# Kernel tuning notes

Measured on AMD Instinct MI355X. Metric: run time of the kernel, lower is better.

Reference implementation:

```python
import jax, jax.numpy as jnp
import numpy as np

N, E, T, D, A = 16384, 65536, 2048, 64, 6


def _w(k, shape, fan_in):
    return jax.random.normal(k, shape, jnp.float32) / np.sqrt(fan_in)


def setup_inputs() -> dict:
    key = jax.random.key(0)
    ks = jax.random.split(key, 20)
    inp = {}
    inp["x"] = jax.random.normal(ks[0], (N, 3), jnp.float32)
    inp["edge_attr"] = jax.random.normal(ks[1], (E, 7), jnp.float32)
    inp["edge_index"] = jax.random.randint(ks[2], (2, E), 0, N)
    inp["nonring"] = jax.random.randint(ks[3], (T, 4), 0, N)
    inp["hx"] = jnp.zeros((1, D), jnp.float32)
    inp["cx"] = jnp.zeros((1, D), jnp.float32)
    inp["W_lin0"] = _w(ks[4], (D, 3), 3); inp["b_lin0"] = jnp.zeros((D,), jnp.float32)
    inp["W_e1"] = _w(ks[5], (128, 7), 7); inp["b_e1"] = jnp.zeros((128,), jnp.float32)
    inp["W_e2"] = _w(ks[6], (D * D, 128), 128); inp["b_e2"] = jnp.zeros((D * D,), jnp.float32)
    inp["conv_root"] = _w(ks[7], (D, D), D); inp["conv_bias"] = jnp.zeros((D,), jnp.float32)
    inp["gru_Wih"] = _w(ks[8], (3 * D, D), D); inp["gru_Whh"] = _w(ks[9], (3 * D, D), D)
    inp["gru_bih"] = jnp.zeros((3 * D,), jnp.float32); inp["gru_bhh"] = jnp.zeros((3 * D,), jnp.float32)
    inp["s2s_Wih"] = _w(ks[10], (4 * D, 2 * D), 2 * D); inp["s2s_Whh"] = _w(ks[11], (4 * D, D), D)
    inp["s2s_bih"] = jnp.zeros((4 * D,), jnp.float32); inp["s2s_bhh"] = jnp.zeros((4 * D,), jnp.float32)
    inp["mem_Wih"] = _w(ks[12], (4 * D, 2 * D), 2 * D); inp["mem_Whh"] = _w(ks[13], (4 * D, D), D)
    inp["mem_bih"] = jnp.zeros((4 * D,), jnp.float32); inp["mem_bhh"] = jnp.zeros((4 * D,), jnp.float32)
    inp["W_lin1"] = _w(ks[14], (D, 5 * D), 5 * D); inp["b_lin1"] = jnp.zeros((D,), jnp.float32)
    inp["W_lin2"] = _w(ks[15], (A, D), D); inp["b_lin2"] = jnp.zeros((A,), jnp.float32)
    inp["W_lin3"] = _w(ks[16], (1, 3 * D), 3 * D); inp["b_lin3"] = jnp.zeros((1,), jnp.float32)
    return inp


def _lstm_cell(xin, h, c, Wih, Whh, bih, bhh):
    g = xin @ Wih.T + bih + h @ Whh.T + bhh
    i, f, gg, o = jnp.split(g, 4, axis=-1)  # torch gate order i,f,g,o
    c = jax.nn.sigmoid(f) * c + jax.nn.sigmoid(i) * jnp.tanh(gg)
    h = jax.nn.sigmoid(o) * jnp.tanh(c)
    return h, c


def _gru_cell(xin, h, Wih, Whh, bih, bhh):
    gi = xin @ Wih.T + bih
    gh = h @ Whh.T + bhh
    ir, iz, inn = jnp.split(gi, 3, axis=-1)  # torch gate order r,z,n
    hr, hz, hn = jnp.split(gh, 3, axis=-1)
    r = jax.nn.sigmoid(ir + hr)
    z = jax.nn.sigmoid(iz + hz)
    n = jnp.tanh(inn + r * hn)
    return (1.0 - z) * n + z * h


def reference(x, edge_attr, edge_index, nonring, hx, cx,
              W_lin0, b_lin0, W_e1, b_e1, W_e2, b_e2, conv_root, conv_bias,
              gru_Wih, gru_Whh, gru_bih, gru_bhh,
              s2s_Wih, s2s_Whh, s2s_bih, s2s_bhh,
              mem_Wih, mem_Whh, mem_bih, mem_bhh,
              W_lin1, b_lin1, W_lin2, b_lin2, W_lin3, b_lin3):
    src, tgt = edge_index[0], edge_index[1]
    out = jax.nn.relu(x @ W_lin0.T + b_lin0)  # [N, D]
    h = out  # GRU hidden (nodes as batch)
    # edge-conditioned dim x dim matrices (NNConv edge MLP)
    ew = jax.nn.relu(edge_attr @ W_e1.T + b_e1)
    ew = (ew @ W_e2.T + b_e2).reshape(E, D, D)  # [E, D, D]
    cnt = jnp.maximum(jax.ops.segment_sum(jnp.ones((E,), out.dtype), tgt, num_segments=N), 1.0)
    for _ in range(3):
        msg = jnp.einsum('ed,edf->ef', out[src], ew)  # per-edge small matmul
        aggr = jax.ops.segment_sum(msg, tgt, num_segments=N) / cnt[:, None]  # scatter-mean
        m = jax.nn.relu(aggr + out @ conv_root + conv_bias)  # NNConv root + bias, then relu
        h = _gru_cell(m, h, gru_Wih, gru_Whh, gru_bih, gru_bhh)
        out = h
    # Set2Set pooling (single graph, B=1), processing_steps=3
    hs = jnp.zeros((1, D), out.dtype)
    cs = jnp.zeros((1, D), out.dtype)
    q_star = jnp.zeros((1, 2 * D), out.dtype)
    for _ in range(3):
        hs, cs = _lstm_cell(q_star, hs, cs, s2s_Wih, s2s_Whh, s2s_bih, s2s_bhh)
        a = jax.nn.softmax(out @ hs[0])  # [N]
        r = (a[:, None] * out).sum(0, keepdims=True)  # [1, D]
        q_star = jnp.concatenate([hs, r], axis=1)
    pool = q_star  # [1, 2D]
    lstm_out, cx_new = _lstm_cell(pool, hx, cx, mem_Wih, mem_Whh, mem_bih, mem_bhh)
    hx_new = lstm_out
    # torsion head: index_select -> view(4*D, -1) -> permute(1,0)
    sel = out[nonring.reshape(-1)]  # [4T, D]
    tfeat = sel.reshape(4 * D, -1).T  # [T, 4D], faithful to torch view semantics
    rep = jnp.repeat(lstm_out.reshape(-1), T).reshape(T, D)  # torch repeat_interleave + view
    pf = jnp.concatenate([tfeat, rep], axis=1)  # [T, 5D]
    logits = jax.nn.relu(pf @ W_lin1.T + b_lin1) @ W_lin2.T + b_lin2  # [T, A]
    v = jnp.concatenate([pool, lstm_out], axis=1) @ W_lin3.T + b_lin3  # [1, 1]
    return logits, v, hx_new, cx_new
```

## Files before the change

kernel.cpp:

```cpp
#include <hip/hip_runtime.h>

#define cN 16384
#define cE 65536
#define cT 2048
#define CAP 78

typedef __attribute__((ext_vector_type(8))) short short8;
typedef __attribute__((ext_vector_type(4))) float f32x4;
typedef __attribute__((ext_vector_type(4))) unsigned u32x4;

__device__ __forceinline__ short f2bf(float f){
  unsigned u = __float_as_uint(f);
  u = (u + 0x7FFFu + ((u >> 16) & 1u)) >> 16;
  return (short)u;
}
__device__ __forceinline__ float bf2f(short s){
  return __uint_as_float(((unsigned)(unsigned short)s) << 16);
}
__device__ __forceinline__ unsigned cvtpk(float lo, float hi){
  unsigned r;
  asm("v_cvt_pk_bf16_f32 %0, %1, %2" : "=v"(r) : "v"(lo), "v"(hi));
  return r;
}
__device__ __forceinline__ float sigm(float x){ return 1.f / (1.f + __expf(-x)); }
__device__ __forceinline__ unsigned fenc(float f){
  unsigned u = __float_as_uint(f);
  return (u & 0x80000000u) ? ~u : (u | 0x80000000u);
}
__device__ __forceinline__ float fdec(unsigned u){
  u = (u & 0x80000000u) ? (u & 0x7FFFFFFFu) : ~u;
  return __uint_as_float(u);
}
__device__ __forceinline__ float wred(float v){
  v += __shfl_xor(v, 32); v += __shfl_xor(v, 16); v += __shfl_xor(v, 8);
  v += __shfl_xor(v, 4);  v += __shfl_xor(v, 2);  v += __shfl_xor(v, 1);
  return v;
}

__global__ __launch_bounds__(256) void k_lin0(const float* __restrict__ x,
    const float* __restrict__ W, const float* __restrict__ b, float* __restrict__ out)
{
  int i = blockIdx.x * 256 + threadIdx.x;
  int n = i >> 6, f = i & 63;
  float acc = b[f] + x[n*3]*W[f*3] + x[n*3+1]*W[f*3+1] + x[n*3+2]*W[f*3+2];
  out[i] = fmaxf(acc, 0.f);
}

__global__ __launch_bounds__(256) void k_h1(const float* __restrict__ ea,
    const float* __restrict__ W, const float* __restrict__ b, short* __restrict__ h1)
{
  int i = blockIdx.x * 256 + threadIdx.x;
  int e = i >> 7, k = i & 127;
  const float* a = ea + e * 7;
  const float* w = W + k * 7;
  float acc = b[k];
  #pragma unroll
  for (int c = 0; c < 7; c++) acc += a[c] * w[c];
  h1[i] = f2bf(fmaxf(acc, 0.f));
}

__global__ __launch_bounds__(256) void k_w2f(const float* __restrict__ W2, short* __restrict__ w2f)
{
  int o = blockIdx.x * 256 + threadIdx.x;
  int j = o & 7, l = (o >> 3) & 63, ks = (o >> 9) & 31, c = (o >> 14) & 7, fb = (o >> 17) & 3;
  int f = fb * 16 + (l & 15);
  int d = c * 8 + j;
  int k = ks * 4 + ((l >> 4) & 3);
  w2f[o] = f2bf(W2[(d * 64 + f) * 128 + k]);
}

__global__ __launch_bounds__(256) void k_b2f(const float* __restrict__ b2, short* __restrict__ b2f)
{
  int o = blockIdx.x * 256 + threadIdx.x;
  int j = o & 7, l = (o >> 3) & 63, ks2 = (o >> 9) & 1, fb = (o >> 10) & 3;
  int d = ks2 * 32 + ((l >> 4) & 3) * 8 + j;
  int f = fb * 16 + (l & 15);
  b2f[o] = f2bf(b2[d * 64 + f]);
}

__global__ __launch_bounds__(256) void k_wpack(const float* __restrict__ convW,
    const float* __restrict__ Wih, const float* __restrict__ Whh, short* __restrict__ wpk)
{
  int o = blockIdx.x * 256 + threadIdx.x;
  int j = o & 7, l = (o >> 3) & 63, kc = (o >> 9) & 1, cb = o >> 10;
  int k = kc * 32 + ((l >> 4) & 3) * 8 + j;
  int c16 = l & 15;
  float v;
  if (cb < 4)       v = convW[k * 64 + cb * 16 + c16];
  else if (cb < 16) v = Wih[((cb - 4) * 16 + c16) * 64 + k];
  else              v = Whh[((cb - 16) * 16 + c16) * 64 + k];
  wpk[o] = f2bf(v);
}

__global__ __launch_bounds__(256) void k_deg(const int* __restrict__ ei, int* __restrict__ deg)
{
  int e = blockIdx.x * 256 + threadIdx.x;
  atomicAdd(&deg[ei[cE + e]], 1);
}

__global__ __launch_bounds__(1024) void k_scan(const int* __restrict__ deg,
    int* __restrict__ rowp, float* __restrict__ cnt)
{
  __shared__ int part[1024];
  int tid = threadIdx.x;
  int base = tid * 16;
  int loc[16]; int s = 0;
  #pragma unroll
  for (int i = 0; i < 16; i++){ loc[i] = s; s += deg[base + i]; }
  part[tid] = s;
  __syncthreads();
  for (int off = 1; off < 1024; off <<= 1){
    int v = (tid >= off) ? part[tid - off] : 0;
    __syncthreads();
    part[tid] += v;
    __syncthreads();
  }
  int inc = part[tid];
  int eb = inc - s;
  #pragma unroll
  for (int i = 0; i < 16; i++){
    rowp[base + i] = eb + loc[i];
    int dv = deg[base + i];
    cnt[base + i] = (float)(dv > 0 ? dv : 1);
  }
  if (tid == 1023) rowp[16384] = inc;
}

__global__ __launch_bounds__(256) void k_scatter(const int* __restrict__ ei,
    const int* __restrict__ rowp, int* __restrict__ cur,
    int* __restrict__ esrc, int* __restrict__ eidx)
{
  int e = blockIdx.x * 256 + threadIdx.x;
  int t = ei[cE + e];
  int pos = rowp[t] + atomicAdd(&cur[t], 1);
  esrc[pos] = ei[e];
  eidx[pos] = e;
}

__global__ __launch_bounds__(256) void k_sagg(const float* __restrict__ out,
    const short* __restrict__ h1, const short* __restrict__ w2f,
    const short* __restrict__ b2f, const int* __restrict__ rowp,
    const int* __restrict__ esrc, const int* __restrict__ eidx,
    float* __restrict__ aggr)
{
  __shared__ __align__(16) short S[16][1040];
  __shared__ __align__(16) unsigned h1i[CAP][64];
  __shared__ __align__(16) float outsf[CAP][64];
  __shared__ __align__(16) short osb[16][72];
  int tid = threadIdx.x, w = tid >> 6, lane = tid & 63;
  int t0 = blockIdx.x * 16;

  int ebase = rowp[t0];
  int eend  = rowp[t0 + 16];
  int ecnt  = eend - ebase;
  bool fits = (ecnt <= CAP);
  int scnt  = fits ? ecnt : CAP;
  for (int i = w; i < scnt; i += 4){
    int eid = eidx[ebase + i];
    int src = esrc[ebase + i];
    unsigned lo = (unsigned short)h1[(size_t)eid * 128 + lane];
    unsigned hi = (unsigned short)h1[(size_t)eid * 128 + 64 + lane];
    h1i[i][lane] = lo | (hi << 16);
    outsf[i][lane] = out[(size_t)src * 64 + lane];
  }
  int toff[4], tcnt[4];
  #pragma unroll
  for (int g = 0; g < 4; g++){
    int t = t0 + w * 4 + g;
    int a = rowp[t], b = rowp[t + 1];
    toff[g] = a - ebase; tcnt[g] = b - a;
  }
  __syncthreads();

  #pragma unroll
  for (int g = 0; g < 4; g++){
    int ti = w * 4 + g;
    float os = 0.f;
    int tf = toff[g], tc = tcnt[g];
    for (int p = 0; p < tc; p++){
      int slot = tf + p;
      if (slot < CAP) os += outsf[slot][lane];
      else            os += out[(size_t)esrc[ebase + slot] * 64 + lane];
    }
    osb[ti][lane] = (short)cvtpk(os, os);
  }

  f32x4 acc = {0.f, 0.f, 0.f, 0.f};
  int arow = lane & 15, kg = lane >> 4;
  for (int c = 0; c < 8; ++c){
    #pragma unroll
    for (int g = 0; g < 4; ++g){
      int ti = w * 4 + g;
      float a0[8], a1[8];
      #pragma unroll
      for (int d = 0; d < 8; d++){ a0[d] = 0.f; a1[d] = 0.f; }
      int tc = tcnt[g], tf = toff[g];
      if (fits){
        #pragma unroll 2
        for (int p = 0; p < tc; ++p){
          int slot = tf + p;
          unsigned u = h1i[slot][lane];
          float h1a = __uint_as_float(u << 16);
          float h1b = __uint_as_float(u & 0xFFFF0000u);
          f32x4 o0 = *(const f32x4*)&outsf[slot][c * 8];
          f32x4 o1 = *(const f32x4*)&outsf[slot][c * 8 + 4];
          a0[0] = fmaf(o0[0], h1a, a0[0]); a1[0] = fmaf(o0[0], h1b, a1[0]);
          a0[1] = fmaf(o0[1], h1a, a0[1]); a1[1] = fmaf(o0[1], h1b, a1[1]);
          a0[2] = fmaf(o0[2], h1a, a0[2]); a1[2] = fmaf(o0[2], h1b, a1[2]);
          a0[3] = fmaf(o0[3], h1a, a0[3]); a1[3] = fmaf(o0[3], h1b, a1[3]);
          a0[4] = fmaf(o1[0], h1a, a0[4]); a1[4] = fmaf(o1[0], h1b, a1[4]);
          a0[5] = fmaf(o1[1], h1a, a0[5]); a1[5] = fmaf(o1[1], h1b, a1[5]);
          a0[6] = fmaf(o1[2], h1a, a0[6]); a1[6] = fmaf(o1[2], h1b, a1[6]);
          a0[7] = fmaf(o1[3], h1a, a0[7]); a1[7] = fmaf(o1[3], h1b, a1[7]);
        }
      } else {
        for (int p = 0; p < tc; ++p){
          int slot = tf + p;
          float h1a, h1b;
          if (slot < CAP){
            unsigned u = h1i[slot][lane];
            h1a = __uint_as_float(u << 16);
            h1b = __uint_as_float(u & 0xFFFF0000u);
            f32x4 o0 = *(const f32x4*)&outsf[slot][c * 8];
            f32x4 o1 = *(const f32x4*)&outsf[slot][c * 8 + 4];
            #pragma unroll
            for (int d = 0; d < 4; d++){
              a0[d] = fmaf(o0[d], h1a, a0[d]); a1[d] = fmaf(o0[d], h1b, a1[d]);
              a0[4+d] = fmaf(o1[d], h1a, a0[4+d]); a1[4+d] = fmaf(o1[d], h1b, a1[4+d]);
            }
          } else {
            int eid = eidx[ebase + slot];
            int src = esrc[ebase + slot];
            h1a = bf2f(h1[(size_t)eid * 128 + lane]);
            h1b = bf2f(h1[(size_t)eid * 128 + 64 + lane]);
            #pragma unroll
            for (int d = 0; d < 8; d++){
              float o = out[(size_t)src * 64 + c * 8 + d];
              a0[d] = fmaf(o, h1a, a0[d]); a1[d] = fmaf(o, h1b, a1[d]);
            }
          }
        }
      }
      u32x4 p0, p1;
      p0[0] = cvtpk(a0[0], a0[1]); p0[1] = cvtpk(a0[2], a0[3]);
      p0[2] = cvtpk(a0[4], a0[5]); p0[3] = cvtpk(a0[6], a0[7]);
      p1[0] = cvtpk(a1[0], a1[1]); p1[1] = cvtpk(a1[2], a1[3]);
      p1[2] = cvtpk(a1[4], a1[5]); p1[3] = cvtpk(a1[6], a1[7]);
      *(u32x4*)&S[ti][lane * 8]       = p0;
      *(u32x4*)&S[ti][512 + lane * 8] = p1;
    }
    __syncthreads();
    const short* bbase = w2f + ((size_t)(w * 8 + c) * 32) * 512 + lane * 8;
    #pragma unroll
    for (int ks = 0; ks < 32; ++ks){
      short8 afr = *(const short8*)&S[arow][ks * 32 + kg * 8];
      short8 bfr = *(const short8*)(bbase + (size_t)ks * 512);
      acc = __builtin_amdgcn_mfma_f32_16x16x32_bf16(afr, bfr, acc, 0, 0, 0);
    }
    __syncthreads();
  }
  #pragma unroll
  for (int ks2 = 0; ks2 < 2; ++ks2){
    short8 osf = *(const short8*)&osb[arow][ks2 * 32 + kg * 8];
    short8 bfr = *(const short8*)(b2f + ((size_t)((w * 2 + ks2) * 64 + lane)) * 8);
    acc = __builtin_amdgcn_mfma_f32_16x16x32_bf16(osf, bfr, acc, 0, 0, 0);
  }
  int fcol = w * 16 + arow;
  int trow = kg * 4;
  #pragma unroll
  for (int q = 0; q < 4; q++)
    aggr[(size_t)(t0 + trow + q) * 64 + fcol] = acc[q];
}

__global__ __launch_bounds__(256) void k_nodeM(float* __restrict__ out,
    const float* __restrict__ aggr, const float* __restrict__ cnt,
    const short* __restrict__ wpk, const float* __restrict__ convB,
    const float* __restrict__ bih, const float* __restrict__ bhh)
{
  __shared__ __align__(16) short outA[64][72];
  __shared__ __align__(16) short mA[64][72];
  __shared__ float sb[448];
  const short8* WF = (const short8*)wpk;
  int tid = threadIdx.x, w = tid >> 6, lane = tid & 63;
  int n0 = blockIdx.x * 64;
  for (int i = tid; i < 2048; i += 256){
    int r = i >> 5, c2 = (i & 31) * 2;
    float2 v = *(const float2*)&out[(size_t)(n0 + r) * 64 + c2];
    *(unsigned*)&outA[r][c2] = cvtpk(v.x, v.y);
  }
  if (tid < 64) sb[tid] = convB[tid];
  for (int i = tid; i < 192; i += 256){ sb[64 + i] = bih[i]; sb[256 + i] = bhh[i]; }
  __syncthreads();
  int arow = lane & 15, kg = lane >> 4;
  int r0 = w * 16;
  short8 aof0 = *(const short8*)&outA[r0 + arow][kg * 8];
  short8 aof1 = *(const short8*)&outA[r0 + arow][32 + kg * 8];
  float ic[4];
  #pragma unroll
  for (int q = 0; q < 4; q++)
    ic[q] = 1.0f / fmaxf(cnt[n0 + r0 + kg * 4 + q], 1.0f);
  #pragma unroll
  for (int cf = 0; cf < 4; cf++){
    f32x4 a = {0.f, 0.f, 0.f, 0.f};
    a = __builtin_amdgcn_mfma_f32_16x16x32_bf16(aof0, WF[(cf * 2 + 0) * 64 + lane], a, 0, 0, 0);
    a = __builtin_amdgcn_mfma_f32_16x16x32_bf16(aof1, WF[(cf * 2 + 1) * 64 + lane], a, 0, 0, 0);
    int col = cf * 16 + arow;
    float cb_ = sb[col];
    #pragma unroll
    for (int q = 0; q < 4; q++){
      int r = n0 + r0 + kg * 4 + q;
      float m = fmaxf(aggr[(size_t)r * 64 + col] * ic[q] + a[q] + cb_, 0.f);
      mA[r0 + kg * 4 + q][col] = f2bf(m);
    }
  }
  __syncthreads();
  short8 amf0 = *(const short8*)&mA[r0 + arow][kg * 8];
  short8 amf1 = *(const short8*)&mA[r0 + arow][32 + kg * 8];
  #pragma unroll
  for (int co = 0; co < 4; co++){
    f32x4 gir = {0,0,0,0}, giz = {0,0,0,0}, gin = {0,0,0,0};
    f32x4 ghr = {0,0,0,0}, ghz = {0,0,0,0}, ghn = {0,0,0,0};
    gir = __builtin_amdgcn_mfma_f32_16x16x32_bf16(amf0, WF[((4  + co) * 2 + 0) * 64 + lane], gir, 0, 0, 0);
    gir = __builtin_amdgcn_mfma_f32_16x16x32_bf16(amf1, WF[((4  + co) * 2 + 1) * 64 + lane], gir, 0, 0, 0);
    giz = __builtin_amdgcn_mfma_f32_16x16x32_bf16(amf0, WF[((8  + co) * 2 + 0) * 64 + lane], giz, 0, 0, 0);
    giz = __builtin_amdgcn_mfma_f32_16x16x32_bf16(amf1, WF[((8  + co) * 2 + 1) * 64 + lane], giz, 0, 0, 0);
    gin = __builtin_amdgcn_mfma_f32_16x16x32_bf16(amf0, WF[((12 + co) * 2 + 0) * 64 + lane], gin, 0, 0, 0);
    gin = __builtin_amdgcn_mfma_f32_16x16x32_bf16(amf1, WF[((12 + co) * 2 + 1) * 64 + lane], gin, 0, 0, 0);
    ghr = __builtin_amdgcn_mfma_f32_16x16x32_bf16(aof0, WF[((16 + co) * 2 + 0) * 64 + lane], ghr, 0, 0, 0);
    ghr = __builtin_amdgcn_mfma_f32_16x16x32_bf16(aof1, WF[((16 + co) * 2 + 1) * 64 + lane], ghr, 0, 0, 0);
    ghz = __builtin_amdgcn_mfma_f32_16x16x32_bf16(aof0, WF[((20 + co) * 2 + 0) * 64 + lane], ghz, 0, 0, 0);
    ghz = __builtin_amdgcn_mfma_f32_16x16x32_bf16(aof1, WF[((20 + co) * 2 + 1) * 64 + lane], ghz, 0, 0, 0);
    ghn = __builtin_amdgcn_mfma_f32_16x16x32_bf16(aof0, WF[((24 + co) * 2 + 0) * 64 + lane], ghn, 0, 0, 0);
    ghn = __builtin_amdgcn_mfma_f32_16x16x32_bf16(aof1, WF[((24 + co) * 2 + 1) * 64 + lane], ghn, 0, 0, 0);
    int col = co * 16 + arow;
    float bir = sb[64 + col],  biz = sb[128 + col], bin_ = sb[192 + col];
    float bhr = sb[256 + col], bhz = sb[320 + col], bhn = sb[384 + col];
    #pragma unroll
    for (int q = 0; q < 4; q++){
      size_t r = (size_t)(n0 + r0 + kg * 4 + q);
      float rr = sigm(gir[q] + bir + ghr[q] + bhr);
      float zz = sigm(giz[q] + biz + ghz[q] + bhz);
      float nn = tanhf(gin[q] + bin_ + rr * (ghn[q] + bhn));
      float o = out[r * 64 + col];
      out[r * 64 + col] = (1.f - zz) * nn + zz * o;
    }
  }
}

__global__ __launch_bounds__(256) void k_dotsF(const float* __restrict__ out,
    const float* __restrict__ Wih, const float* __restrict__ Whh,
    const float* __restrict__ bih, const float* __restrict__ bhh,
    float* __restrict__ scal, float* __restrict__ sbuf, int st)
{
  __shared__ float q[128];
  __shared__ float hsL[64];
  __shared__ float gsh[4][64];
  __shared__ float hsh[64];
  __shared__ float smax[4];
  const float* pg = scal + st * 256;
  float* pn = scal + (st + 1) * 256;
  int tid = threadIdx.x, gg = tid >> 6, lane = tid & 63;
  if (gg == 0){
    float hs = pg[lane];
    float es = pg[193];
    float rv = (es == 0.f) ? 0.f : pg[128 + lane] / es;
    q[lane] = hs; q[64 + lane] = rv; hsL[lane] = hs;
  }
  __syncthreads();
  float2 fq = *(const float2*)&q[2 * lane];
  float hv0 = hsL[lane];
  #pragma unroll 4
  for (int o = 0; o < 64; o++){
    int row = gg * 64 + o;
    float2 wv = *(const float2*)&Wih[(size_t)row * 128 + 2 * lane];
    float s = wv.x * fq.x + wv.y * fq.y + Whh[(size_t)row * 64 + lane] * hv0;
    s = wred(s);
    if (lane == 0) gsh[gg][o] = s;
  }
  __syncthreads();
  if (gg == 0){
    float gi = gsh[0][lane] + bih[lane]       + bhh[lane];
    float gf = gsh[1][lane] + bih[64 + lane]  + bhh[64 + lane];
    float gv = gsh[2][lane] + bih[128 + lane] + bhh[128 + lane];
    float go = gsh[3][lane] + bih[192 + lane] + bhh[192 + lane];
    float cs = pg[64 + lane];
    float cn = sigm(gf) * cs + sigm(gi) * tanhf(gv);
    float hn = sigm(go) * tanhf(cn);
    hsh[lane] = hn;
    if (blockIdx.x == 0){ pn[lane] = hn; pn[64 + lane] = cn; }
  }
  __syncthreads();
  int nbase = blockIdx.x * 64 + gg * 16;
  float hv = hsh[lane];
  float wmax = -3.4e38f;
  #pragma unroll 4
  for (int i = 0; i < 16; i++){
    int n = nbase + i;
    float p = wred(out[(size_t)n * 64 + lane] * hv);
    if (lane == 0) sbuf[n] = p;
    wmax = fmaxf(wmax, p);
  }
  if (lane == 0) smax[gg] = wmax;
  __syncthreads();
  if (tid == 0){
    float m = fmaxf(fmaxf(smax[0], smax[1]), fmaxf(smax[2], smax[3]));
    atomicMax((unsigned*)(pn + 192), fenc(m));
  }
}

__global__ __launch_bounds__(256) void k_smF(const float* __restrict__ out,
    const float* __restrict__ sbuf, float* __restrict__ scal, int st)
{
  float* pn = scal + (st + 1) * 256;
  __shared__ float ebuf[64];
  __shared__ float rpart[4][64];
  int tid = threadIdx.x, wid = tid >> 6, lane = tid & 63;
  float gm = fdec(((const unsigned*)pn)[192]);
  int n0 = blockIdx.x * 64;
  if (tid < 64) ebuf[tid] = __expf(sbuf[n0 + tid] - gm);
  __syncthreads();
  float racc = 0.f;
  #pragma unroll 4
  for (int i = 0; i < 16; i++){
    int idx = wid * 16 + i;
    racc += ebuf[idx] * out[(size_t)(n0 + idx) * 64 + lane];
  }
  rpart[wid][lane] = racc;
  __syncthreads();
  if (wid == 0){
    float rt = rpart[0][lane] + rpart[1][lane] + rpart[2][lane] + rpart[3][lane];
    atomicAdd(&pn[128 + lane], rt);
  } else if (wid == 1){
    float es = wred(ebuf[lane]);
    if (lane == 0) atomicAdd(&pn[193], es);
  }
}

__global__ __launch_bounds__(256) void k_memlstm(const float* __restrict__ Wih,
    const float* __restrict__ Whh, const float* __restrict__ bih,
    const float* __restrict__ bhh, const float* __restrict__ hx,
    const float* __restrict__ cx, const float* __restrict__ W3,
    const float* __restrict__ b3, float* __restrict__ scal, float* __restrict__ dout)
{
  __shared__ float pool[128];
  __shared__ float hxs[64];
  __shared__ float gsh[4][64];
  __shared__ float lob[64];
  const float* pg = scal + 3 * 256;
  int tid = threadIdx.x, gg = tid >> 6, lane = tid & 63;
  if (gg == 0){
    pool[lane] = pg[lane];
    pool[64 + lane] = pg[128 + lane] / pg[193];
    hxs[lane] = hx[lane];
  }
  __syncthreads();
  float2 fq = *(const float2*)&pool[2 * lane];
  float hv = hxs[lane];
  #pragma unroll 4
  for (int o = 0; o < 64; o++){
    int row = gg * 64 + o;
    float2 wv = *(const float2*)&Wih[(size_t)row * 128 + 2 * lane];
    float s = wv.x * fq.x + wv.y * fq.y + Whh[(size_t)row * 64 + lane] * hv;
    s = wred(s);
    if (lane == 0) gsh[gg][o] = s;
  }
  __syncthreads();
  if (gg == 0){
    float gi = gsh[0][lane] + bih[lane]       + bhh[lane];
    float gf = gsh[1][lane] + bih[64 + lane]  + bhh[64 + lane];
    float gv = gsh[2][lane] + bih[128 + lane] + bhh[128 + lane];
    float go = gsh[3][lane] + bih[192 + lane] + bhh[192 + lane];
    float cn = sigm(gf) * cx[lane] + sigm(gi) * tanhf(gv);
    float hn = sigm(go) * tanhf(cn);
    dout[12289 + lane] = hn;
    dout[12353 + lane] = cn;
    scal[1024 + lane] = hn;
    lob[lane] = hn;
  }
  __syncthreads();
  if (gg == 0){
    float a = pool[lane] * W3[lane] + pool[64 + lane] * W3[64 + lane]
            + lob[lane] * W3[128 + lane];
    a = wred(a);
    if (lane == 0) dout[12288] = a + b3[0];
  }
}

__global__ __launch_bounds__(256) void k_head(const float* __restrict__ out,
    const int* __restrict__ nr, const float* __restrict__ scal,
    const float* __restrict__ W1, const float* __restrict__ b1,
    const float* __restrict__ W2, const float* __restrict__ b2,
    float* __restrict__ dout)
{
  __shared__ float pf[4][320];
  __shared__ float hb[4][64];
  int tid = threadIdx.x, wid = tid >> 6, lane = tid & 63;
  int t = blockIdx.x * 4 + wid;
  float lo = scal[1024 + (t >> 5)];
  #pragma unroll
  for (int rep = 0; rep < 4; rep++){
    int j = rep * 64 + lane;
    int idx = nr[j * 32 + (t >> 6)];
    pf[wid][j] = out[idx * 64 + (t & 63)];
  }
  pf[wid][256 + lane] = lo;
  __syncthreads();
  float acc = b1[lane];
  const float* w = W1 + lane * 320;
  #pragma unroll 4
  for (int j = 0; j < 320; j++) acc += pf[wid][j] * w[j];
  hb[wid][lane] = fmaxf(acc, 0.f);
  __syncthreads();
  if (lane < 6){
    float a2 = b2[lane];
    const float* w2 = W2 + lane * 64;
    #pragma unroll 4
    for (int f = 0; f < 64; f++) a2 += hb[wid][f] * w2[f];
    dout[t * 6 + lane] = a2;
  }
}

extern "C" void kernel_launch(void* const* d_in, const int* in_sizes, int n_in,
                              void* d_out, int out_size, void* d_ws, size_t ws_size,
                              hipStream_t stream)
{
  const float* x         = (const float*)d_in[0];
  const float* edge_attr = (const float*)d_in[1];
  const int*   ei        = (const int*)d_in[2];
  const int*   nonring   = (const int*)d_in[3];
  const float* hx        = (const float*)d_in[4];
  const float* cx        = (const float*)d_in[5];
  const float* W_lin0 = (const float*)d_in[6];  const float* b_lin0 = (const float*)d_in[7];
  const float* W_e1   = (const float*)d_in[8];  const float* b_e1   = (const float*)d_in[9];
  const float* W_e2   = (const float*)d_in[10]; const float* b_e2   = (const float*)d_in[11];
  const float* convW  = (const float*)d_in[12]; const float* convB  = (const float*)d_in[13];
  const float* gWih   = (const float*)d_in[14]; const float* gWhh   = (const float*)d_in[15];
  const float* gbih   = (const float*)d_in[16]; const float* gbhh   = (const float*)d_in[17];
  const float* sWih   = (const float*)d_in[18]; const float* sWhh   = (const float*)d_in[19];
  const float* sbih   = (const float*)d_in[20]; const float* sbhh   = (const float*)d_in[21];
  const float* mWih   = (const float*)d_in[22]; const float* mWhh   = (const float*)d_in[23];
  const float* mbih   = (const float*)d_in[24]; const float* mbhh   = (const float*)d_in[25];
  const float* W_lin1 = (const float*)d_in[26]; const float* b_lin1 = (const float*)d_in[27];
  const float* W_lin2 = (const float*)d_in[28]; const float* b_lin2 = (const float*)d_in[29];
  const float* W_lin3 = (const float*)d_in[30]; const float* b_lin3 = (const float*)d_in[31];
  float* dout = (float*)d_out;

  char* w = (char*)d_ws;
  float* outb = (float*)w;  w += (size_t)cN * 64 * 4;
  float* aggr = (float*)w;  w += (size_t)cN * 64 * 4;
  short* h1   = (short*)w;  w += (size_t)cE * 128 * 2;
  short* w2f  = (short*)w;  w += (size_t)64 * 8192 * 2;
  short* b2f  = (short*)w;  w += 4096 * 2;
  short* wpk  = (short*)w;  w += 28672 * 2;
  float* cntb = (float*)w;  w += cN * 4;
  float* sbuf = (float*)w;  w += cN * 4;
  float* scal = (float*)w;  w += 1088 * 4;
  int* deg  = (int*)w;  w += cN * 4;
  int* cur  = (int*)w;  w += cN * 4;
  int* rowp = (int*)w;  w += (cN + 1) * 4 + 60;
  int* esrc = (int*)w;  w += cE * 4;
  int* eidx = (int*)w;  w += cE * 4;

  hipMemsetAsync(deg, 0, cN * 4, stream);
  hipMemsetAsync(cur, 0, cN * 4, stream);
  hipMemsetAsync(scal, 0, 1088 * 4, stream);

  k_lin0<<<cN * 64 / 256, 256, 0, stream>>>(x, W_lin0, b_lin0, outb);
  k_h1<<<cE * 128 / 256, 256, 0, stream>>>(edge_attr, W_e1, b_e1, h1);
  k_w2f<<<64 * 8192 / 256, 256, 0, stream>>>(W_e2, w2f);
  k_b2f<<<16, 256, 0, stream>>>(b_e2, b2f);
  k_wpack<<<112, 256, 0, stream>>>(convW, gWih, gWhh, wpk);
  k_deg<<<cE / 256, 256, 0, stream>>>(ei, deg);
  k_scan<<<1, 1024, 0, stream>>>(deg, rowp, cntb);
  k_scatter<<<cE / 256, 256, 0, stream>>>(ei, rowp, cur, esrc, eidx);

  for (int it = 0; it < 3; it++){
    k_sagg<<<cN / 16, 256, 0, stream>>>(outb, h1, w2f, b2f, rowp, esrc, eidx, aggr);
    k_nodeM<<<cN / 64, 256, 0, stream>>>(outb, aggr, cntb, wpk, convB, gbih, gbhh);
  }

  for (int st = 0; st < 3; st++){
    k_dotsF<<<cN / 64, 256, 0, stream>>>(outb, sWih, sWhh, sbih, sbhh, scal, sbuf, st);
    k_smF<<<cN / 64, 256, 0, stream>>>(outb, sbuf, scal, st);
  }

  k_memlstm<<<1, 256, 0, stream>>>(mWih, mWhh, mbih, mbhh, hx, cx, W_lin3, b_lin3, scal, dout);
  k_head<<<cT / 4, 256, 0, stream>>>(outb, nonring, scal, W_lin1, b_lin1, W_lin2, b_lin2, dout);
}
```

Before: 601.4 us.

## Double sagg tile with bf16 staged features; restructure set2set softmax as two-level reduction

k_sagg now processes 32 targets per block with 512 threads. It raises the LDS edge cache capacity and stores the gathered source features as packed bf16 to halve LDS use. The Set2Set softmax drops the global atomicMax plus second pass over node features. Each block now computes a local max, the exp-sum and the weighted partial sum from an LDS tile, and a single-block kernel rescales and combines the partials and, on the last step, runs the memory LSTM. This removes one full pass over the node features and the separate k_memlstm launch, at the cost of extra bf16 rounding of features in the aggregation and a serial single-block reduction.

```diff
diff --git a/kernel.cpp b/kernel.cpp
--- a/kernel.cpp
+++ b/kernel.cpp
@@ -3,7 +3,7 @@
 #define cN 16384
 #define cE 65536
 #define cT 2048
-#define CAP 78
+#define CAP 168
 
 typedef __attribute__((ext_vector_type(8))) short short8;
 typedef __attribute__((ext_vector_type(4))) float f32x4;
@@ -23,17 +23,15 @@
   return r;
 }
 __device__ __forceinline__ float sigm(float x){ return 1.f / (1.f + __expf(-x)); }
-__device__ __forceinline__ unsigned fenc(float f){
-  unsigned u = __float_as_uint(f);
-  return (u & 0x80000000u) ? ~u : (u | 0x80000000u);
-}
-__device__ __forceinline__ float fdec(unsigned u){
-  u = (u & 0x80000000u) ? (u & 0x7FFFFFFFu) : ~u;
-  return __uint_as_float(u);
-}
 __device__ __forceinline__ float wred(float v){
   v += __shfl_xor(v, 32); v += __shfl_xor(v, 16); v += __shfl_xor(v, 8);
   v += __shfl_xor(v, 4);  v += __shfl_xor(v, 2);  v += __shfl_xor(v, 1);
+  return v;
+}
+__device__ __forceinline__ float wredmax(float v){
+  v = fmaxf(v, __shfl_xor(v, 32)); v = fmaxf(v, __shfl_xor(v, 16));
+  v = fmaxf(v, __shfl_xor(v, 8));  v = fmaxf(v, __shfl_xor(v, 4));
+  v = fmaxf(v, __shfl_xor(v, 2));  v = fmaxf(v, __shfl_xor(v, 1));
   return v;
 }
 
@@ -137,31 +135,34 @@
   eidx[pos] = e;
 }
 
-__global__ __launch_bounds__(256) void k_sagg(const float* __restrict__ out,
+__global__ __launch_bounds__(512) void k_sagg(const float* __restrict__ out,
     const short* __restrict__ h1, const short* __restrict__ w2f,
     const short* __restrict__ b2f, const int* __restrict__ rowp,
     const int* __restrict__ esrc, const int* __restrict__ eidx,
     float* __restrict__ aggr)
 {
-  __shared__ __align__(16) short S[16][1040];
+  __shared__ __align__(16) short S[32][1040];
   __shared__ __align__(16) unsigned h1i[CAP][64];
-  __shared__ __align__(16) float outsf[CAP][64];
-  __shared__ __align__(16) short osb[16][72];
+  __shared__ __align__(16) unsigned outsp[CAP][32];
+  __shared__ __align__(16) short osb[32][72];
   int tid = threadIdx.x, w = tid >> 6, lane = tid & 63;
-  int t0 = blockIdx.x * 16;
+  int t0 = blockIdx.x * 32;
 
   int ebase = rowp[t0];
-  int eend  = rowp[t0 + 16];
+  int eend  = rowp[t0 + 32];
   int ecnt  = eend - ebase;
   bool fits = (ecnt <= CAP);
   int scnt  = fits ? ecnt : CAP;
-  for (int i = w; i < scnt; i += 4){
+  for (int i = w; i < scnt; i += 8){
     int eid = eidx[ebase + i];
     int src = esrc[ebase + i];
     unsigned lo = (unsigned short)h1[(size_t)eid * 128 + lane];
     unsigned hi = (unsigned short)h1[(size_t)eid * 128 + 64 + lane];
     h1i[i][lane] = lo | (hi << 16);
-    outsf[i][lane] = out[(size_t)src * 64 + lane];
+    if (lane < 32){
+      float2 v = *(const float2*)&out[(size_t)src * 64 + lane * 2];
+      outsp[i][lane] = cvtpk(v.x, v.y);
+    }
   }
   int toff[4], tcnt[4];
   #pragma unroll
@@ -179,14 +180,19 @@
     int tf = toff[g], tc = tcnt[g];
     for (int p = 0; p < tc; p++){
       int slot = tf + p;
-      if (slot < CAP) os += outsf[slot][lane];
-      else            os += out[(size_t)esrc[ebase + slot] * 64 + lane];
+      if (slot < CAP){
+        unsigned u = outsp[slot][lane >> 1];
+        os += __uint_as_float((lane & 1) ? (u & 0xFFFF0000u) : (u << 16));
+      } else {
+        os += out[(size_t)esrc[ebase + slot] * 64 + lane];
+      }
     }
     osb[ti][lane] = (short)cvtpk(os, os);
   }
 
   f32x4 acc = {0.f, 0.f, 0.f, 0.f};
   int arow = lane & 15, kg = lane >> 4;
+  int rb = w >> 2, fb = w & 3;
   for (int c = 0; c < 8; ++c){
     #pragma unroll
     for (int g = 0; g < 4; ++g){
@@ -202,37 +208,40 @@
           unsigned u = h1i[slot][lane];
           float h1a = __uint_as_float(u << 16);
           float h1b = __uint_as_float(u & 0xFFFF0000u);
-          f32x4 o0 = *(const f32x4*)&outsf[slot][c * 8];
-          f32x4 o1 = *(const f32x4*)&outsf[slot][c * 8 + 4];
-          a0[0] = fmaf(o0[0], h1a, a0[0]); a1[0] = fmaf(o0[0], h1b, a1[0]);
-          a0[1] = fmaf(o0[1], h1a, a0[1]); a1[1] = fmaf(o0[1], h1b, a1[1]);
-          a0[2] = fmaf(o0[2], h1a, a0[2]); a1[2] = fmaf(o0[2], h1b, a1[2]);
-          a0[3] = fmaf(o0[3], h1a, a0[3]); a1[3] = fmaf(o0[3], h1b, a1[3]);
-          a0[4] = fmaf(o1[0], h1a, a0[4]); a1[4] = fmaf(o1[0], h1b, a1[4]);
-          a0[5] = fmaf(o1[1], h1a, a0[5]); a1[5] = fmaf(o1[1], h1b, a1[5]);
-          a0[6] = fmaf(o1[2], h1a, a0[6]); a1[6] = fmaf(o1[2], h1b, a1[6]);
-          a0[7] = fmaf(o1[3], h1a, a0[7]); a1[7] = fmaf(o1[3], h1b, a1[7]);
+          u32x4 ov = *(const u32x4*)&outsp[slot][c * 4];
+          float o0 = __uint_as_float(ov[0] << 16), o1 = __uint_as_float(ov[0] & 0xFFFF0000u);
+          float o2 = __uint_as_float(ov[1] << 16), o3 = __uint_as_float(ov[1] & 0xFFFF0000u);
+          float o4 = __uint_as_float(ov[2] << 16), o5 = __uint_as_float(ov[2] & 0xFFFF0000u);
+          float o6 = __uint_as_float(ov[3] << 16), o7 = __uint_as_float(ov[3] & 0xFFFF0000u);
+          a0[0] = fmaf(o0, h1a, a0[0]); a1[0] = fmaf(o0, h1b, a1[0]);
+          a0[1] = fmaf(o1, h1a, a0[1]); a1[1] = fmaf(o1, h1b, a1[1]);
+          a0[2] = fmaf(o2, h1a, a0[2]); a1[2] = fmaf(o2, h1b, a1[2]);
+          a0[3] = fmaf(o3, h1a, a0[3]); a1[3] = fmaf(o3, h1b, a1[3]);
+          a0[4] = fmaf(o4, h1a, a0[4]); a1[4] = fmaf(o4, h1b, a1[4]);
+          a0[5] = fmaf(o5, h1a, a0[5]); a1[5] = fmaf(o5, h1b, a1[5]);
+          a0[6] = fmaf(o6, h1a, a0[6]); a1[6] = fmaf(o6, h1b, a1[6]);
+          a0[7] = fmaf(o7, h1a, a0[7]); a1[7] = fmaf(o7, h1b, a1[7]);
         }
       } else {
         for (int p = 0; p < tc; ++p){
           int slot = tf + p;
-          float h1a, h1b;
           if (slot < CAP){
             unsigned u = h1i[slot][lane];
-            h1a = __uint_as_float(u << 16);
-            h1b = __uint_as_float(u & 0xFFFF0000u);
-            f32x4 o0 = *(const f32x4*)&outsf[slot][c * 8];
-            f32x4 o1 = *(const f32x4*)&outsf[slot][c * 8 + 4];
+            float h1a = __uint_as_float(u << 16);
+            float h1b = __uint_as_float(u & 0xFFFF0000u);
+            u32x4 ov = *(const u32x4*)&outsp[slot][c * 4];
             #pragma unroll
             for (int d = 0; d < 4; d++){
-              a0[d] = fmaf(o0[d], h1a, a0[d]); a1[d] = fmaf(o0[d], h1b, a1[d]);
-              a0[4+d] = fmaf(o1[d], h1a, a0[4+d]); a1[4+d] = fmaf(o1[d], h1b, a1[4+d]);
+              float lo = __uint_as_float(ov[d] << 16);
+              float hi = __uint_as_float(ov[d] & 0xFFFF0000u);
+              a0[2*d]   = fmaf(lo, h1a, a0[2*d]);   a1[2*d]   = fmaf(lo, h1b, a1[2*d]);
+              a0[2*d+1] = fmaf(hi, h1a, a0[2*d+1]); a1[2*d+1] = fmaf(hi, h1b, a1[2*d+1]);
             }
           } else {
             int eid = eidx[ebase + slot];
             int src = esrc[ebase + slot];
-            h1a = bf2f(h1[(size_t)eid * 128 + lane]);
-            h1b = bf2f(h1[(size_t)eid * 128 + 64 + lane]);
+            float h1a = bf2f(h1[(size_t)eid * 128 + lane]);
+            float h1b = bf2f(h1[(size_t)eid * 128 + 64 + lane]);
             #pragma unroll
             for (int d = 0; d < 8; d++){
               float o = out[(size_t)src * 64 + c * 8 + d];
@@ -250,10 +259,10 @@
       *(u32x4*)&S[ti][512 + lane * 8] = p1;
     }
     __syncthreads();
-    const short* bbase = w2f + ((size_t)(w * 8 + c) * 32) * 512 + lane * 8;
+    const short* bbase = w2f + ((size_t)(fb * 8 + c) * 32) * 512 + lane * 8;
     #pragma unroll
     for (int ks = 0; ks < 32; ++ks){
-      short8 afr = *(const short8*)&S[arow][ks * 32 + kg * 8];
+      short8 afr = *(const short8*)&S[rb * 16 + arow][ks * 32 + kg * 8];
       short8 bfr = *(const short8*)(bbase + (size_t)ks * 512);
       acc = __builtin_amdgcn_mfma_f32_16x16x32_bf16(afr, bfr, acc, 0, 0, 0);
     }
@@ -261,12 +270,12 @@
   }
   #pragma unroll
   for (int ks2 = 0; ks2 < 2; ++ks2){
-    short8 osf = *(const short8*)&osb[arow][ks2 * 32 + kg * 8];
-    short8 bfr = *(const short8*)(b2f + ((size_t)((w * 2 + ks2) * 64 + lane)) * 8);
+    short8 osf = *(const short8*)&osb[rb * 16 + arow][ks2 * 32 + kg * 8];
+    short8 bfr = *(const short8*)(b2f + ((size_t)((fb * 2 + ks2) * 64 + lane)) * 8);
     acc = __builtin_amdgcn_mfma_f32_16x16x32_bf16(osf, bfr, acc, 0, 0, 0);
   }
-  int fcol = w * 16 + arow;
-  int trow = kg * 4;
+  int fcol = fb * 16 + arow;
+  int trow = rb * 16 + kg * 4;
   #pragma unroll
   for (int q = 0; q < 4; q++)
     aggr[(size_t)(t0 + trow + q) * 64 + fcol] = acc[q];
@@ -350,13 +359,18 @@
 __global__ __launch_bounds__(256) void k_dotsF(const float* __restrict__ out,
     const float* __restrict__ Wih, const float* __restrict__ Whh,
     const float* __restrict__ bih, const float* __restrict__ bhh,
-    float* __restrict__ scal, float* __restrict__ sbuf, int st)
+    float* __restrict__ scal, float* __restrict__ rbuf,
+    float* __restrict__ bmbuf, float* __restrict__ esbuf, int st)
 {
   __shared__ float q[128];
   __shared__ float hsL[64];
   __shared__ float gsh[4][64];
   __shared__ float hsh[64];
   __shared__ float smax[4];
+  __shared__ float otile[64][64];
+  __shared__ float sarr[64];
+  __shared__ float ebuf[64];
+  __shared__ float rpart[4][64];
   const float* pg = scal + st * 256;
   float* pn = scal + (st + 1) * 256;
   int tid = threadIdx.x, gg = tid >> 6, lane = tid & 63;
@@ -395,94 +409,110 @@
   float wmax = -3.4e38f;
   #pragma unroll 4
   for (int i = 0; i < 16; i++){
-    int n = nbase + i;
-    float p = wred(out[(size_t)n * 64 + lane] * hv);
-    if (lane == 0) sbuf[n] = p;
+    float v = out[(size_t)(nbase + i) * 64 + lane];
+    otile[gg * 16 + i][lane] = v;
+    float p = wred(v * hv);
+    if (lane == 0) sarr[gg * 16 + i] = p;
     wmax = fmaxf(wmax, p);
   }
   if (lane == 0) smax[gg] = wmax;
   __syncthreads();
-  if (tid == 0){
-    float m = fmaxf(fmaxf(smax[0], smax[1]), fmaxf(smax[2], smax[3]));
-    atomicMax((unsigned*)(pn + 192), fenc(m));
-  }
-}
-
-__global__ __launch_bounds__(256) void k_smF(const float* __restrict__ out,
-    const float* __restrict__ sbuf, float* __restrict__ scal, int st)
-{
-  float* pn = scal + (st + 1) * 256;
-  __shared__ float ebuf[64];
-  __shared__ float rpart[4][64];
-  int tid = threadIdx.x, wid = tid >> 6, lane = tid & 63;
-  float gm = fdec(((const unsigned*)pn)[192]);
-  int n0 = blockIdx.x * 64;
-  if (tid < 64) ebuf[tid] = __expf(sbuf[n0 + tid] - gm);
+  float bm = fmaxf(fmaxf(smax[0], smax[1]), fmaxf(smax[2], smax[3]));
+  if (tid < 64) ebuf[tid] = __expf(sarr[tid] - bm);
   __syncthreads();
   float racc = 0.f;
   #pragma unroll 4
-  for (int i = 0; i < 16; i++){
-    int idx = wid * 16 + i;
-    racc += ebuf[idx] * out[(size_t)(n0 + idx) * 64 + lane];
-  }
-  rpart[wid][lane] = racc;
-  __syncthreads();
-  if (wid == 0){
-    float rt = rpart[0][lane] + rpart[1][lane] + rpart[2][lane] + rpart[3][lane];
-    atomicAdd(&pn[128 + lane], rt);
-  } else if (wid == 1){
+  for (int i = 0; i < 16; i++)
+    racc += ebuf[gg * 16 + i] * otile[gg * 16 + i][lane];
+  rpart[gg][lane] = racc;
+  __syncthreads();
+  if (gg == 0){
+    float r = rpart[0][lane] + rpart[1][lane] + rpart[2][lane] + rpart[3][lane];
+    rbuf[blockIdx.x * 64 + lane] = r;
+  } else if (gg == 1){
     float es = wred(ebuf[lane]);
-    if (lane == 0) atomicAdd(&pn[193], es);
-  }
-}
-
-__global__ __launch_bounds__(256) void k_memlstm(const float* __restrict__ Wih,
-    const float* __restrict__ Whh, const float* __restrict__ bih,
-    const float* __restrict__ bhh, const float* __restrict__ hx,
-    const float* __restrict__ cx, const float* __restrict__ W3,
-    const float* __restrict__ b3, float* __restrict__ scal, float* __restrict__ dout)
-{
+    if (lane == 0) esbuf[blockIdx.x] = es;
+  } else if (gg == 2 && lane == 0) bmbuf[blockIdx.x] = bm;
+}
+
+__global__ __launch_bounds__(256) void k_smF(const float* __restrict__ rbuf,
+    const float* __restrict__ bmbuf, const float* __restrict__ esbuf,
+    float* __restrict__ scal, int st,
+    const float* __restrict__ Wih, const float* __restrict__ Whh,
+    const float* __restrict__ bih, const float* __restrict__ bhh,
+    const float* __restrict__ hx, const float* __restrict__ cx,
+    const float* __restrict__ W3, const float* __restrict__ b3,
+    float* __restrict__ dout)
+{
+  __shared__ float redA[4], redB[4];
+  __shared__ float rpart[4][64];
+  __shared__ float rr[64];
   __shared__ float pool[128];
   __shared__ float hxs[64];
   __shared__ float gsh[4][64];
   __shared__ float lob[64];
-  const float* pg = scal + 3 * 256;
-  int tid = threadIdx.x, gg = tid >> 6, lane = tid & 63;
-  if (gg == 0){
-    pool[lane] = pg[lane];
-    pool[64 + lane] = pg[128 + lane] / pg[193];
-    hxs[lane] = hx[lane];
-  }
-  __syncthreads();
-  float2 fq = *(const float2*)&pool[2 * lane];
-  float hv = hxs[lane];
-  #pragma unroll 4
-  for (int o = 0; o < 64; o++){
-    int row = gg * 64 + o;
-    float2 wv = *(const float2*)&Wih[(size_t)row * 128 + 2 * lane];
-    float s = wv.x * fq.x + wv.y * fq.y + Whh[(size_t)row * 64 + lane] * hv;
-    s = wred(s);
-    if (lane == 0) gsh[gg][o] = s;
-  }
-  __syncthreads();
-  if (gg == 0){
-    float gi = gsh[0][lane] + bih[lane]       + bhh[lane];
-    float gf = gsh[1][lane] + bih[64 + lane]  + bhh[64 + lane];
-    float gv = gsh[2][lane] + bih[128 + lane] + bhh[128 + lane];
-    float go = gsh[3][lane] + bih[192 + lane] + bhh[192 + lane];
-    float cn = sigm(gf) * cx[lane] + sigm(gi) * tanhf(gv);
-    float hn = sigm(go) * tanhf(cn);
-    dout[12289 + lane] = hn;
-    dout[12353 + lane] = cn;
-    scal[1024 + lane] = hn;
-    lob[lane] = hn;
-  }
-  __syncthreads();
-  if (gg == 0){
-    float a = pool[lane] * W3[lane] + pool[64 + lane] * W3[64 + lane]
-            + lob[lane] * W3[128 + lane];
-    a = wred(a);
-    if (lane == 0) dout[12288] = a + b3[0];
+  int tid = threadIdx.x, wid = tid >> 6, lane = tid & 63;
+  float* pn = scal + (st + 1) * 256;
+  float bm = bmbuf[tid];
+  float m = wredmax(bm);
+  if (lane == 0) redA[wid] = m;
+  __syncthreads();
+  float gmax = fmaxf(fmaxf(redA[0], redA[1]), fmaxf(redA[2], redA[3]));
+  float ep = __expf(bm - gmax) * esbuf[tid];
+  float es = wred(ep);
+  if (lane == 0) redB[wid] = es;
+  float racc = 0.f;
+  for (int i = 0; i < 64; i++){
+    int b = wid * 64 + i;
+    racc += __expf(bmbuf[b] - gmax) * rbuf[b * 64 + lane];
+  }
+  rpart[wid][lane] = racc;
+  __syncthreads();
+  float esum = redB[0] + redB[1] + redB[2] + redB[3];
+  if (wid == 0){
+    float r = rpart[0][lane] + rpart[1][lane] + rpart[2][lane] + rpart[3][lane];
+    rr[lane] = r;
+    pn[128 + lane] = r;
+  }
+  if (tid == 0) pn[193] = esum;
+  if (st == 2){
+    __syncthreads();
+    if (wid == 0){
+      pool[lane] = pn[lane];
+      pool[64 + lane] = rr[lane] / esum;
+      hxs[lane] = hx[lane];
+    }
+    __syncthreads();
+    float2 fq = *(const float2*)&pool[2 * lane];
+    float hv = hxs[lane];
+    #pragma unroll 4
+    for (int o = 0; o < 64; o++){
+      int row = wid * 64 + o;
+      float2 wv = *(const float2*)&Wih[(size_t)row * 128 + 2 * lane];
+      float s = wv.x * fq.x + wv.y * fq.y + Whh[(size_t)row * 64 + lane] * hv;
+      s = wred(s);
+      if (lane == 0) gsh[wid][o] = s;
+    }
+    __syncthreads();
+    if (wid == 0){
+      float gi = gsh[0][lane] + bih[lane]       + bhh[lane];
+      float gf = gsh[1][lane] + bih[64 + lane]  + bhh[64 + lane];
+      float gv = gsh[2][lane] + bih[128 + lane] + bhh[128 + lane];
+      float go = gsh[3][lane] + bih[192 + lane] + bhh[192 + lane];
+      float cn = sigm(gf) * cx[lane] + sigm(gi) * tanhf(gv);
+      float hn = sigm(go) * tanhf(cn);
+      dout[12289 + lane] = hn;
+      dout[12353 + lane] = cn;
+      scal[1024 + lane] = hn;
+      lob[lane] = hn;
+    }
+    __syncthreads();
+    if (wid == 0){
+      float a = pool[lane] * W3[lane] + pool[64 + lane] * W3[64 + lane]
+              + lob[lane] * W3[128 + lane];
+      a = wred(a);
+      if (lane == 0) dout[12288] = a + b3[0];
+    }
   }
 }
 
@@ -553,7 +583,9 @@
   short* b2f  = (short*)w;  w += 4096 * 2;
   short* wpk  = (short*)w;  w += 28672 * 2;
   float* cntb = (float*)w;  w += cN * 4;
-  float* sbuf = (float*)w;  w += cN * 4;
+  float* rbuf = (float*)w;  w += 256 * 64 * 4;
+  float* bmbuf= (float*)w;  w += 256 * 4;
+  float* esbuf= (float*)w;  w += 256 * 4;
   float* scal = (float*)w;  w += 1088 * 4;
   int* deg  = (int*)w;  w += cN * 4;
   int* cur  = (int*)w;  w += cN * 4;
@@ -575,15 +607,15 @@
   k_scatter<<<cE / 256, 256, 0, stream>>>(ei, rowp, cur, esrc, eidx);
 
   for (int it = 0; it < 3; it++){
-    k_sagg<<<cN / 16, 256, 0, stream>>>(outb, h1, w2f, b2f, rowp, esrc, eidx, aggr);
+    k_sagg<<<cN / 32, 512, 0, stream>>>(outb, h1, w2f, b2f, rowp, esrc, eidx, aggr);
     k_nodeM<<<cN / 64, 256, 0, stream>>>(outb, aggr, cntb, wpk, convB, gbih, gbhh);
   }
 
   for (int st = 0; st < 3; st++){
-    k_dotsF<<<cN / 64, 256, 0, stream>>>(outb, sWih, sWhh, sbih, sbhh, scal, sbuf, st);
-    k_smF<<<cN / 64, 256, 0, stream>>>(outb, sbuf, scal, st);
-  }
-
-  k_memlstm<<<1, 256, 0, stream>>>(mWih, mWhh, mbih, mbhh, hx, cx, W_lin3, b_lin3, scal, dout);
+    k_dotsF<<<cN / 64, 256, 0, stream>>>(outb, sWih, sWhh, sbih, sbhh, scal, rbuf, bmbuf, esbuf, st);
+    k_smF<<<1, 256, 0, stream>>>(rbuf, bmbuf, esbuf, scal, st,
+                                 mWih, mWhh, mbih, mbhh, hx, cx, W_lin3, b_lin3, dout);
+  }
+
   k_head<<<cT / 4, 256, 0, stream>>>(outb, nonring, scal, W_lin1, b_lin1, W_lin2, b_lin2, dout);
 }
```

Result: slower. 656.3 us (+9.1%).
